# Kernel optimization log

Measured on AMD Instinct MI355X. Metric: run time of the kernel, lower is better.

Reference implementation:

```python
import jax, jax.numpy as jnp
import numpy as np

B, A, OBS, NACT, H, D = 8192, 8, 128, 32, 256, 64  # batch, n_agents, obs_shape, n_actions, rnn_hidden_dim, attn_dim
N = B * A


def setup_inputs() -> dict:
    key = jax.random.key(0)
    ks = jax.random.split(key, 12)
    s = 0.02
    return {
        "o": jax.random.normal(ks[0], (N, OBS), dtype=jnp.float32),
        "o_next": jax.random.normal(ks[1], (N, OBS), dtype=jnp.float32),
        "h": jax.random.normal(ks[2], (N, H), dtype=jnp.float32),
        "actions": jax.random.uniform(ks[3], (N, A, NACT), dtype=jnp.float32),
        "wq_w": jax.random.normal(ks[4], (D, 2 * OBS), dtype=jnp.float32) * s,
        "wq_b": jnp.zeros((D,), dtype=jnp.float32),
        "wk_w": jax.random.normal(ks[5], (D, NACT), dtype=jnp.float32) * s,
        "wk_b": jnp.zeros((D,), dtype=jnp.float32),
        "wv1_w": jax.random.normal(ks[6], (D, H + NACT), dtype=jnp.float32) * s,
        "wv1_b": jnp.zeros((D,), dtype=jnp.float32),
        "wv2_w": jax.random.normal(ks[7], (NACT, D), dtype=jnp.float32) * s,
        "wv2_b": jnp.zeros((NACT,), dtype=jnp.float32),
    }


def reference(o, o_next, h, actions, wq_w, wq_b, wk_w, wk_b, wv1_w, wv1_b, wv2_w, wv2_b):
    n, a, nact = actions.shape           # [N, A, n_actions]
    d = wq_w.shape[0]                    # attn_dim
    hdim = h.shape[-1]
    b = n // a
    # query: [N, D]
    query = jnp.concatenate([o, o_next], axis=-1) @ wq_w.T + wq_b
    # key: [N, A, D]
    key = (actions.reshape(-1, nact) @ wk_w.T + wk_b).reshape(n, a, d)
    # value: repeat h per attended agent -> [B*A*A, H]
    h_rep = jnp.tile(h.reshape(b, a, hdim), (1, a, 1)).reshape(-1, hdim)
    inps_v = jnp.concatenate([h_rep, actions.reshape(-1, nact)], axis=-1)
    hid = jax.nn.relu(inps_v @ wv1_w.T + wv1_b)
    value = (hid @ wv2_w.T + wv2_b).reshape(n, a, nact)
    # attention scores with self-masked diagonal
    scale = 1.0 / (float(d) ** 0.5)
    scores = jnp.einsum('nd,nad->na', query * scale, key).reshape(b, a, a)
    eye = jnp.eye(a, dtype=bool)
    scores = jnp.where(eye[None, :, :], jnp.asarray(-1e9, scores.dtype), scores)
    attn = jax.nn.softmax(scores, axis=-1).reshape(n, a, 1)
    q = jnp.sum(value * attn, axis=1)    # [N, n_actions]
    return q
```

## Files before the change

### kernel.cpp

```cpp
#include <hip/hip_runtime.h>
#include <hip/hip_bf16.h>

typedef __attribute__((ext_vector_type(8))) short bf16x8;
typedef __attribute__((ext_vector_type(4))) float f32x4;

#define MFMA(A, B, C) __builtin_amdgcn_mfma_f32_16x16x32_bf16((A), (B), (C), 0, 0, 0)
#define SB() __builtin_amdgcn_sched_barrier(0)

#define OFF_TB    0
#define OFF_WT_H  128
#define OFF_WT_L  16512
#define OFF_WHV_H 32896
#define OFF_WHV_L 65664
#define OFF_WA_H  98432
#define OFF_WA_L  102528

#define SM_HV   0
#define SM_AT   4352
#define SM_SS   4864
#define SM_TOT  7168

__device__ __forceinline__ unsigned short f2bf(float v) {
    unsigned u = __builtin_bit_cast(unsigned, v);
    return (unsigned short)((u + 0x7fffu + ((u >> 16) & 1u)) >> 16);
}
__device__ __forceinline__ float bf2f(unsigned short b) {
    return __builtin_bit_cast(float, ((unsigned)b) << 16);
}
__device__ __forceinline__ ushort2 splitf(float v) {
    unsigned short h = f2bf(v);
    unsigned short l = f2bf(v - bf2f(h));
    return make_ushort2(h, l);
}

__device__ __forceinline__ unsigned as_u32(__hip_bfloat162 v) {
    unsigned u;
    __builtin_memcpy(&u, &v, sizeof(u));
    return u;
}
__device__ __forceinline__ unsigned pk2(float x, float y) {
    return as_u32(__float22bfloat162_rn(make_float2(x, y)));
}
__device__ __forceinline__ bf16x8 cvt8(float4 a, float4 b) {
    uint4 H;
    H.x = pk2(a.x, a.y);
    H.y = pk2(a.z, a.w);
    H.z = pk2(b.x, b.y);
    H.w = pk2(b.z, b.w);
    return __builtin_bit_cast(bf16x8, H);
}

__global__ __launch_bounds__(256) void k_setup(const float* __restrict__ wq_w,
                                               const float* __restrict__ wq_b,
                                               const float* __restrict__ wk_w,
                                               const float* __restrict__ wv1,
                                               char* __restrict__ ws) {
    int gid = blockIdx.x * 256 + threadIdx.x;
    if (gid < 8192) {
        int k = gid >> 8, c = gid & 255;
        float acc = 0.f;
#pragma unroll 8
        for (int d = 0; d < 64; ++d) acc = fmaf(wk_w[d * 32 + k], wq_w[d * 256 + c], acc);
        ushort2 s = splitf(0.125f * acc);
        ((unsigned short*)(ws + OFF_WT_H))[gid] = s.x;
        ((unsigned short*)(ws + OFF_WT_L))[gid] = s.y;
    } else if (gid < 24576) {
        int i = gid - 8192;
        ushort2 s = splitf(wv1[(i >> 8) * 288 + (i & 255)]);
        ((unsigned short*)(ws + OFF_WHV_H))[i] = s.x;
        ((unsigned short*)(ws + OFF_WHV_L))[i] = s.y;
    } else if (gid < 26624) {
        int i = gid - 24576;
        ushort2 s = splitf(wv1[(i >> 5) * 288 + 256 + (i & 31)]);
        ((unsigned short*)(ws + OFF_WA_H))[i] = s.x;
        ((unsigned short*)(ws + OFF_WA_L))[i] = s.y;
    } else if (gid < 26656) {
        int k = gid - 26624;
        float b = 0.f;
#pragma unroll 8
        for (int d = 0; d < 64; ++d) b = fmaf(wk_w[d * 32 + k], wq_b[d], b);
        ((float*)(ws + OFF_TB))[k] = 0.125f * b;
    }
}

__global__ __launch_bounds__(64, 4) void fused(
    const float* __restrict__ o, const float* __restrict__ onx,
    const float* __restrict__ h, const float* __restrict__ act,
    const float* __restrict__ wv1b, const float* __restrict__ wv2,
    const float* __restrict__ wv2b, const char* __restrict__ ws,
    float* __restrict__ out)
{
    __shared__ __align__(16) char sm[SM_TOT];
    float* HV = (float*)(sm + SM_HV);
    float* AT = (float*)(sm + SM_AT);
    unsigned short* SS = (unsigned short*)(sm + SM_SS);

    const int lane = threadIdx.x;
    const int l15  = lane & 15;
    const int quad = lane >> 4;
    const int n0   = blockIdx.x * 16;
    const int myrow = n0 + l15;

    const f32x4 zv = {0.f, 0.f, 0.f, 0.f};
    f32x4 acc_hv[4] = {zv, zv, zv, zv};
    f32x4 acc_t[2]  = {zv, zv};

    bf16x8 Bx[8];

    {
        float4 xa[8], xb[8];
#pragma unroll
        for (int ch = 0; ch < 8; ++ch) {
            const float* src = (ch < 4)
                ? o   + (size_t)myrow * 128 + ch * 32 + quad * 8
                : onx + (size_t)myrow * 128 + (ch - 4) * 32 + quad * 8;
            xa[ch] = ((const float4*)src)[0];
            xb[ch] = ((const float4*)src)[1];
        }
        SB();
#pragma unroll
        for (int ch = 0; ch < 8; ++ch) Bx[ch] = cvt8(xa[ch], xb[ch]);
    }
#pragma unroll
    for (int mt = 0; mt < 2; ++mt) {
        bf16x8 wf[8];
#pragma unroll
        for (int ch = 0; ch < 8; ++ch)
            wf[ch] = *(const bf16x8*)(ws + OFF_WT_H +
                     (((mt * 16 + l15) * 256) + ch * 32 + quad * 8) * 2);
        SB();
#pragma unroll
        for (int ch = 0; ch < 8; ++ch) acc_t[mt] = MFMA(wf[ch], Bx[ch], acc_t[mt]);
    }

    {
        float4 xa[8], xb[8];
#pragma unroll
        for (int ch = 0; ch < 8; ++ch) {
            const float* src = h + (size_t)myrow * 256 + ch * 32 + quad * 8;
            xa[ch] = ((const float4*)src)[0];
            xb[ch] = ((const float4*)src)[1];
        }
        SB();
#pragma unroll
        for (int ch = 0; ch < 8; ++ch) Bx[ch] = cvt8(xa[ch], xb[ch]);
    }
#pragma unroll
    for (int mt = 0; mt < 4; ++mt) {
        bf16x8 wf[8];
#pragma unroll
        for (int ch = 0; ch < 8; ++ch)
            wf[ch] = *(const bf16x8*)(ws + OFF_WHV_H +
                     (((mt * 16 + l15) * 256) + ch * 32 + quad * 8) * 2);
        SB();
#pragma unroll
        for (int ch = 0; ch < 8; ++ch) acc_hv[mt] = MFMA(wf[ch], Bx[ch], acc_hv[mt]);
    }

    const float* arow = act + (size_t)myrow * 256;
    float4 av0[8], av1[8];
#pragma unroll
    for (int j = 0; j < 8; ++j) {
        av0[j] = *(const float4*)(arow + j * 32 + quad * 4);
        av1[j] = *(const float4*)(arow + j * 32 + 16 + quad * 4);
    }
    SB();

#pragma unroll
    for (int mt = 0; mt < 4; ++mt) {
        int d0 = mt * 16 + quad * 4;
        float4 b = *(const float4*)&wv1b[d0];
        f32x4 a = acc_hv[mt];
        *(float4*)&HV[l15 * 68 + d0] =
            make_float4(a[0] + b.x, a[1] + b.y, a[2] + b.z, a[3] + b.w);
    }

    {
        float t8[8];
        const float* tb = (const float*)(ws + OFF_TB);
#pragma unroll
        for (int mt = 0; mt < 2; ++mt) {
            float4 b = *(const float4*)&tb[mt * 16 + quad * 4];
            t8[mt * 4 + 0] = acc_t[mt][0] + b.x;
            t8[mt * 4 + 1] = acc_t[mt][1] + b.y;
            t8[mt * 4 + 2] = acc_t[mt][2] + b.z;
            t8[mt * 4 + 3] = acc_t[mt][3] + b.w;
        }
        float sc[8];
#pragma unroll
        for (int j = 0; j < 8; ++j) {
            float s = 0.f;
            s = fmaf(t8[0], av0[j].x, s);
            s = fmaf(t8[1], av0[j].y, s);
            s = fmaf(t8[2], av0[j].z, s);
            s = fmaf(t8[3], av0[j].w, s);
            s = fmaf(t8[4], av1[j].x, s);
            s = fmaf(t8[5], av1[j].y, s);
            s = fmaf(t8[6], av1[j].z, s);
            s = fmaf(t8[7], av1[j].w, s);
            sc[j] = s;
        }
#pragma unroll
        for (int j = 0; j < 8; ++j) {
            sc[j] += __shfl_xor(sc[j], 16);
            sc[j] += __shfl_xor(sc[j], 32);
        }
        const int diag = l15 & 7;
        float mx = -1e30f;
#pragma unroll
        for (int j = 0; j < 8; ++j) if (j != diag) mx = fmaxf(mx, sc[j]);
        float ex[8], sum = 0.f;
#pragma unroll
        for (int j = 0; j < 8; ++j) {
            ex[j] = (j == diag) ? 0.f : __expf(sc[j] - mx);
            sum += ex[j];
        }
        float inv = 1.f / sum;
        if (quad == 0) {
            *(float4*)&AT[l15 * 8] =
                make_float4(ex[0] * inv, ex[1] * inv, ex[2] * inv, ex[3] * inv);
            *(float4*)&AT[l15 * 8 + 4] =
                make_float4(ex[4] * inv, ex[5] * inv, ex[6] * inv, ex[7] * inv);
        }
    }

    const int jB  = l15 & 7;
    const int nbh = l15 >> 3;
    bf16x8 WAh[4];
#pragma unroll
    for (int mt = 0; mt < 4; ++mt) {
        int off = ((mt * 16 + l15) * 32 + quad * 8) * 2;
        WAh[mt] = *(const bf16x8*)(ws + OFF_WA_H + off);
    }
    float4 bv0a[4], bv0b[4];
#pragma unroll
    for (int ii = 0; ii < 4; ++ii) {
        int nb = ii * 2 + nbh;
        const float* ap = act + (size_t)(n0 + nb) * 256 + jB * 32 + quad * 8;
        bv0a[ii] = ((const float4*)ap)[0];
        bv0b[ii] = ((const float4*)ap)[1];
    }
    SB();
    __syncthreads();

    float4 bv1a[4], bv1b[4];
#pragma unroll
    for (int ii = 0; ii < 4; ++ii) {
        int nb = (4 + ii) * 2 + nbh;
        const float* ap = act + (size_t)(n0 + nb) * 256 + jB * 32 + quad * 8;
        bv1a[ii] = ((const float4*)ap)[0];
        bv1b[ii] = ((const float4*)ap)[1];
    }
    SB();

#pragma unroll
    for (int half = 0; half < 2; ++half) {
#pragma unroll
        for (int ii = 0; ii < 4; ++ii) {
            int nb = (half * 4 + ii) * 2 + nbh;
            bf16x8 Bh = (half == 0) ? cvt8(bv0a[ii], bv0b[ii])
                                    : cvt8(bv1a[ii], bv1b[ii]);
            f32x4 accB[4] = {zv, zv, zv, zv};
#pragma unroll
            for (int mt = 0; mt < 4; ++mt)
                accB[mt] = MFMA(WAh[mt], Bh, accB[mt]);
            int hrow = (nb & 8) + jB;
            float at = AT[nb * 8 + jB];
#pragma unroll
            for (int mt = 0; mt < 4; ++mt) {
                int d0 = mt * 16 + quad * 4;
                float4 hv4 = *(const float4*)&HV[hrow * 68 + d0];
                float r0 = at * fmaxf(accB[mt][0] + hv4.x, 0.f);
                float r1 = at * fmaxf(accB[mt][1] + hv4.y, 0.f);
                float r2 = at * fmaxf(accB[mt][2] + hv4.z, 0.f);
                float r3 = at * fmaxf(accB[mt][3] + hv4.w, 0.f);
#pragma unroll
                for (int m = 1; m <= 4; m <<= 1) {
                    r0 += __shfl_xor(r0, m);
                    r1 += __shfl_xor(r1, m);
                    r2 += __shfl_xor(r2, m);
                    r3 += __shfl_xor(r3, m);
                }
                if (jB == 0)
                    *(uint2*)&SS[nb * 72 + d0] = make_uint2(pk2(r0, r1), pk2(r2, r3));
            }
        }
        if (half == 0) SB();
    }

    float4 wva[4], wvb[4];
#pragma unroll
    for (int c = 0; c < 4; ++c) {
        const float* wp = wv2 + ((c >> 1) * 16 + l15) * 64 + (c & 1) * 32 + quad * 8;
        wva[c] = ((const float4*)wp)[0];
        wvb[c] = ((const float4*)wp)[1];
    }
    SB();
    __syncthreads();

    {
        bf16x8 Sb[2];
#pragma unroll
        for (int kc = 0; kc < 2; ++kc)
            Sb[kc] = *(const bf16x8*)&SS[l15 * 72 + kc * 32 + quad * 8];
        f32x4 acc2[2] = {zv, zv};
#pragma unroll
        for (int c = 0; c < 4; ++c) {
            bf16x8 Ah = cvt8(wva[c], wvb[c]);
            acc2[c >> 1] = MFMA(Ah, Sb[c & 1], acc2[c >> 1]);
        }
#pragma unroll
        for (int et = 0; et < 2; ++et) {
            int e0 = et * 16 + quad * 4;
            float4 b = *(const float4*)&wv2b[e0];
            f32x4 a = acc2[et];
            *(float4*)&out[(size_t)(n0 + l15) * 32 + e0] =
                make_float4(a[0] + b.x, a[1] + b.y, a[2] + b.z, a[3] + b.w);
        }
    }
}

extern "C" void kernel_launch(void* const* d_in, const int* in_sizes, int n_in,
                              void* d_out, int out_size, void* d_ws, size_t ws_size,
                              hipStream_t stream) {
    const float* o     = (const float*)d_in[0];
    const float* onx   = (const float*)d_in[1];
    const float* h     = (const float*)d_in[2];
    const float* act   = (const float*)d_in[3];
    const float* wq_w  = (const float*)d_in[4];
    const float* wq_b  = (const float*)d_in[5];
    const float* wk_w  = (const float*)d_in[6];
    const float* wv1_w = (const float*)d_in[8];
    const float* wv1_b = (const float*)d_in[9];
    const float* wv2_w = (const float*)d_in[10];
    const float* wv2_b = (const float*)d_in[11];
    float* out = (float*)d_out;
    char* ws   = (char*)d_ws;

    k_setup<<<105, 256, 0, stream>>>(wq_w, wq_b, wk_w, wv1_w, ws);
    fused<<<4096, 64, 0, stream>>>(o, onx, h, act, wv1_b, wv2_w, wv2_b, ws, out);
}
```

Baseline: 236.2 us.

## Use inline-asm global loads with explicit vmcnt waits to control load scheduling

Replaces compiler-generated vector loads with inline-asm global_load_dwordx4 instructions and explicit s_waitcnt vmcnt(0) barriers, taking control of where loads are issued and where they are awaited. It also splits the actions-row loads into two halves so the second half is in flight while scores for the first half are computed, and hoists bias loads earlier. The aim is to overlap memory latency with compute across stages. The risk is that volatile asm with a full vmcnt(0) wait serialises every outstanding load and hides them from the compiler's scheduler, and the reads issued before __syncthreads now stay outstanding across the barrier.

New measurement: 235.7 us. No clear change (-0.2%).

```diff
diff --git a/kernel.cpp b/kernel.cpp
--- a/kernel.cpp
+++ b/kernel.cpp
@@ -5,7 +5,6 @@
 typedef __attribute__((ext_vector_type(4))) float f32x4;
 
 #define MFMA(A, B, C) __builtin_amdgcn_mfma_f32_16x16x32_bf16((A), (B), (C), 0, 0, 0)
-#define SB() __builtin_amdgcn_sched_barrier(0)
 
 #define OFF_TB    0
 #define OFF_WT_H  128
@@ -41,13 +40,33 @@
 __device__ __forceinline__ unsigned pk2(float x, float y) {
     return as_u32(__float22bfloat162_rn(make_float2(x, y)));
 }
-__device__ __forceinline__ bf16x8 cvt8(float4 a, float4 b) {
+__device__ __forceinline__ bf16x8 cvt8(f32x4 a, f32x4 b) {
     uint4 H;
-    H.x = pk2(a.x, a.y);
-    H.y = pk2(a.z, a.w);
-    H.z = pk2(b.x, b.y);
-    H.w = pk2(b.z, b.w);
+    H.x = pk2(a[0], a[1]);
+    H.y = pk2(a[2], a[3]);
+    H.z = pk2(b[0], b[1]);
+    H.w = pk2(b[2], b[3]);
     return __builtin_bit_cast(bf16x8, H);
+}
+
+__device__ __forceinline__ f32x4 gld(const float* p) {
+    f32x4 r;
+    asm volatile("global_load_dwordx4 %0, %1, off" : "=v"(r) : "v"(p));
+    return r;
+}
+__device__ __forceinline__ f32x4 gldo16(const float* p) {
+    f32x4 r;
+    asm volatile("global_load_dwordx4 %0, %1, off offset:16" : "=v"(r) : "v"(p));
+    return r;
+}
+__device__ __forceinline__ bf16x8 gldw(const void* p) {
+    bf16x8 r;
+    asm volatile("global_load_dwordx4 %0, %1, off" : "=v"(r) : "v"(p));
+    return r;
+}
+__device__ __forceinline__ void vmwait() {
+    asm volatile("s_waitcnt vmcnt(0)" ::: "memory");
+    __builtin_amdgcn_sched_barrier(0);
 }
 
 __global__ __launch_bounds__(256) void k_setup(const float* __restrict__ wq_w,
@@ -108,16 +127,16 @@
     bf16x8 Bx[8];
 
     {
-        float4 xa[8], xb[8];
+        f32x4 xa[8], xb[8];
 #pragma unroll
         for (int ch = 0; ch < 8; ++ch) {
             const float* src = (ch < 4)
                 ? o   + (size_t)myrow * 128 + ch * 32 + quad * 8
                 : onx + (size_t)myrow * 128 + (ch - 4) * 32 + quad * 8;
-            xa[ch] = ((const float4*)src)[0];
-            xb[ch] = ((const float4*)src)[1];
-        }
-        SB();
+            xa[ch] = gld(src);
+            xb[ch] = gldo16(src);
+        }
+        vmwait();
 #pragma unroll
         for (int ch = 0; ch < 8; ++ch) Bx[ch] = cvt8(xa[ch], xb[ch]);
     }
@@ -126,22 +145,21 @@
         bf16x8 wf[8];
 #pragma unroll
         for (int ch = 0; ch < 8; ++ch)
-            wf[ch] = *(const bf16x8*)(ws + OFF_WT_H +
-                     (((mt * 16 + l15) * 256) + ch * 32 + quad * 8) * 2);
-        SB();
+            wf[ch] = gldw(ws + OFF_WT_H + (((mt * 16 + l15) * 256) + ch * 32 + quad * 8) * 2);
+        vmwait();
 #pragma unroll
         for (int ch = 0; ch < 8; ++ch) acc_t[mt] = MFMA(wf[ch], Bx[ch], acc_t[mt]);
     }
 
     {
-        float4 xa[8], xb[8];
+        f32x4 xa[8], xb[8];
 #pragma unroll
         for (int ch = 0; ch < 8; ++ch) {
             const float* src = h + (size_t)myrow * 256 + ch * 32 + quad * 8;
-            xa[ch] = ((const float4*)src)[0];
-            xb[ch] = ((const float4*)src)[1];
-        }
-        SB();
+            xa[ch] = gld(src);
+            xb[ch] = gldo16(src);
+        }
+        vmwait();
 #pragma unroll
         for (int ch = 0; ch < 8; ++ch) Bx[ch] = cvt8(xa[ch], xb[ch]);
     }
@@ -150,56 +168,70 @@
         bf16x8 wf[8];
 #pragma unroll
         for (int ch = 0; ch < 8; ++ch)
-            wf[ch] = *(const bf16x8*)(ws + OFF_WHV_H +
-                     (((mt * 16 + l15) * 256) + ch * 32 + quad * 8) * 2);
-        SB();
+            wf[ch] = gldw(ws + OFF_WHV_H + (((mt * 16 + l15) * 256) + ch * 32 + quad * 8) * 2);
+        vmwait();
 #pragma unroll
         for (int ch = 0; ch < 8; ++ch) acc_hv[mt] = MFMA(wf[ch], Bx[ch], acc_hv[mt]);
     }
 
     const float* arow = act + (size_t)myrow * 256;
-    float4 av0[8], av1[8];
-#pragma unroll
-    for (int j = 0; j < 8; ++j) {
-        av0[j] = *(const float4*)(arow + j * 32 + quad * 4);
-        av1[j] = *(const float4*)(arow + j * 32 + 16 + quad * 4);
-    }
-    SB();
+    const float* tbp  = (const float*)(ws + OFF_TB);
+    f32x4 b4[4], tb0, tb1, av0[8], av1[8];
+#pragma unroll
+    for (int mt = 0; mt < 4; ++mt) b4[mt] = gld(&wv1b[mt * 16 + quad * 4]);
+    tb0 = gld(tbp + quad * 4);
+    tb1 = gld(tbp + 16 + quad * 4);
+#pragma unroll
+    for (int j = 0; j < 4; ++j) {
+        av0[j] = gld(arow + j * 32 + quad * 4);
+        av1[j] = gld(arow + j * 32 + 16 + quad * 4);
+    }
+    vmwait();
 
 #pragma unroll
     for (int mt = 0; mt < 4; ++mt) {
         int d0 = mt * 16 + quad * 4;
-        float4 b = *(const float4*)&wv1b[d0];
         f32x4 a = acc_hv[mt];
         *(float4*)&HV[l15 * 68 + d0] =
-            make_float4(a[0] + b.x, a[1] + b.y, a[2] + b.z, a[3] + b.w);
-    }
-
+            make_float4(a[0] + b4[mt][0], a[1] + b4[mt][1],
+                        a[2] + b4[mt][2], a[3] + b4[mt][3]);
+    }
+
+    float sc[8];
     {
         float t8[8];
-        const float* tb = (const float*)(ws + OFF_TB);
-#pragma unroll
-        for (int mt = 0; mt < 2; ++mt) {
-            float4 b = *(const float4*)&tb[mt * 16 + quad * 4];
-            t8[mt * 4 + 0] = acc_t[mt][0] + b.x;
-            t8[mt * 4 + 1] = acc_t[mt][1] + b.y;
-            t8[mt * 4 + 2] = acc_t[mt][2] + b.z;
-            t8[mt * 4 + 3] = acc_t[mt][3] + b.w;
-        }
-        float sc[8];
-#pragma unroll
-        for (int j = 0; j < 8; ++j) {
+#pragma unroll
+        for (int r = 0; r < 4; ++r) {
+            t8[r]     = acc_t[0][r] + tb0[r];
+            t8[4 + r] = acc_t[1][r] + tb1[r];
+        }
+#pragma unroll
+        for (int j = 4; j < 8; ++j) {
+            av0[j] = gld(arow + j * 32 + quad * 4);
+            av1[j] = gld(arow + j * 32 + 16 + quad * 4);
+        }
+#pragma unroll
+        for (int j = 0; j < 4; ++j) {
             float s = 0.f;
-            s = fmaf(t8[0], av0[j].x, s);
-            s = fmaf(t8[1], av0[j].y, s);
-            s = fmaf(t8[2], av0[j].z, s);
-            s = fmaf(t8[3], av0[j].w, s);
-            s = fmaf(t8[4], av1[j].x, s);
-            s = fmaf(t8[5], av1[j].y, s);
-            s = fmaf(t8[6], av1[j].z, s);
-            s = fmaf(t8[7], av1[j].w, s);
+            s = fmaf(t8[0], av0[j][0], s); s = fmaf(t8[1], av0[j][1], s);
+            s = fmaf(t8[2], av0[j][2], s); s = fmaf(t8[3], av0[j][3], s);
+            s = fmaf(t8[4], av1[j][0], s); s = fmaf(t8[5], av1[j][1], s);
+            s = fmaf(t8[6], av1[j][2], s); s = fmaf(t8[7], av1[j][3], s);
             sc[j] = s;
         }
+        vmwait();
+#pragma unroll
+        for (int j = 4; j < 8; ++j) {
+            float s = 0.f;
+            s = fmaf(t8[0], av0[j][0], s); s = fmaf(t8[1], av0[j][1], s);
+            s = fmaf(t8[2], av0[j][2], s); s = fmaf(t8[3], av0[j][3], s);
+            s = fmaf(t8[4], av1[j][0], s); s = fmaf(t8[5], av1[j][1], s);
+            s = fmaf(t8[6], av1[j][2], s); s = fmaf(t8[7], av1[j][3], s);
+            sc[j] = s;
+        }
+    }
+
+    {
 #pragma unroll
         for (int j = 0; j < 8; ++j) {
             sc[j] += __shfl_xor(sc[j], 16);
@@ -228,30 +260,26 @@
     const int nbh = l15 >> 3;
     bf16x8 WAh[4];
 #pragma unroll
-    for (int mt = 0; mt < 4; ++mt) {
-        int off = ((mt * 16 + l15) * 32 + quad * 8) * 2;
-        WAh[mt] = *(const bf16x8*)(ws + OFF_WA_H + off);
-    }
-    float4 bv0a[4], bv0b[4];
+    for (int mt = 0; mt < 4; ++mt)
+        WAh[mt] = gldw(ws + OFF_WA_H + ((mt * 16 + l15) * 32 + quad * 8) * 2);
+    f32x4 bv0a[4], bv0b[4];
 #pragma unroll
     for (int ii = 0; ii < 4; ++ii) {
         int nb = ii * 2 + nbh;
         const float* ap = act + (size_t)(n0 + nb) * 256 + jB * 32 + quad * 8;
-        bv0a[ii] = ((const float4*)ap)[0];
-        bv0b[ii] = ((const float4*)ap)[1];
-    }
-    SB();
+        bv0a[ii] = gld(ap);
+        bv0b[ii] = gldo16(ap);
+    }
     __syncthreads();
-
-    float4 bv1a[4], bv1b[4];
+    f32x4 bv1a[4], bv1b[4];
 #pragma unroll
     for (int ii = 0; ii < 4; ++ii) {
         int nb = (4 + ii) * 2 + nbh;
         const float* ap = act + (size_t)(n0 + nb) * 256 + jB * 32 + quad * 8;
-        bv1a[ii] = ((const float4*)ap)[0];
-        bv1b[ii] = ((const float4*)ap)[1];
-    }
-    SB();
+        bv1a[ii] = gld(ap);
+        bv1b[ii] = gldo16(ap);
+    }
+    vmwait();
 
 #pragma unroll
     for (int half = 0; half < 2; ++half) {
@@ -285,17 +313,15 @@
                     *(uint2*)&SS[nb * 72 + d0] = make_uint2(pk2(r0, r1), pk2(r2, r3));
             }
         }
-        if (half == 0) SB();
-    }
-
-    float4 wva[4], wvb[4];
+    }
+
+    f32x4 wva[4], wvb[4];
 #pragma unroll
     for (int c = 0; c < 4; ++c) {
         const float* wp = wv2 + ((c >> 1) * 16 + l15) * 64 + (c & 1) * 32 + quad * 8;
-        wva[c] = ((const float4*)wp)[0];
-        wvb[c] = ((const float4*)wp)[1];
-    }
-    SB();
+        wva[c] = gld(wp);
+        wvb[c] = gldo16(wp);
+    }
     __syncthreads();
 
     {
@@ -303,6 +329,7 @@
 #pragma unroll
         for (int kc = 0; kc < 2; ++kc)
             Sb[kc] = *(const bf16x8*)&SS[l15 * 72 + kc * 32 + quad * 8];
+        vmwait();
         f32x4 acc2[2] = {zv, zv};
 #pragma unroll
         for (int c = 0; c < 4; ++c) {
```
